# Optimization experiments

Hardware: AMD Instinct MI355X
Metric: run time of the kernel (lower is better)

The kernel has to match this reference:

```python
import jax, jax.numpy as jnp
import numpy as np

NUM_HEADS = 16
ROPE_THETA = 10000.0


def apply_rope(x, positions):
    # x: [B, H, S, D], positions: [S] int
    d = x.shape[-1]
    inv_freq = ROPE_THETA ** (-jnp.arange(0, d, 2, dtype=jnp.float32) / d)  # [D/2]
    ang = positions.astype(jnp.float32)[:, None] * inv_freq[None, :]        # [S, D/2]
    cos, sin = jnp.cos(ang), jnp.sin(ang)                                   # [S, D/2]
    x1, x2 = x[..., 0::2], x[..., 1::2]                                     # even/odd pairs
    r1 = x1 * cos - x2 * sin
    r2 = x1 * sin + x2 * cos
    return jnp.stack([r1, r2], axis=-1).reshape(x.shape)


def setup_inputs() -> dict:
    key = jax.random.key(0)
    k1, k2, k3 = jax.random.split(key, 3)
    B, S, D = 2, 2048, 2048
    x = jax.random.normal(k1, (B, S, D), dtype=jnp.float32)
    token_positions = jnp.arange(S, dtype=jnp.int64)
    w_qkv = jax.random.normal(k2, (D, 3 * D), dtype=jnp.float32) * (D ** -0.5)
    w_o = jax.random.normal(k3, (D, D), dtype=jnp.float32) * (D ** -0.5)
    return {"x": x, "token_positions": token_positions, "w_qkv": w_qkv, "w_o": w_o}


def reference(x, token_positions, w_qkv, w_o):
    B, S, D = x.shape
    H = NUM_HEADS
    hd = D // H
    qkv = x @ w_qkv                                   # [B, S, 3D]
    qkv = qkv.reshape(B, S, 3, H, hd)                 # split '(r h d)'
    q = jnp.transpose(qkv[:, :, 0], (0, 2, 1, 3))     # [B, H, S, hd]
    k = jnp.transpose(qkv[:, :, 1], (0, 2, 1, 3))
    v = jnp.transpose(qkv[:, :, 2], (0, 2, 1, 3))
    q = apply_rope(q, token_positions)
    k = apply_rope(k, token_positions)
    scale = 1.0 / jnp.sqrt(jnp.float32(hd))
    scores = jnp.einsum('bhqd,bhkd->bhqk', q, k) * scale  # [B, H, S, S]
    causal = jnp.tril(jnp.ones((S, S), dtype=bool))
    scores = jnp.where(causal[None, None], scores, jnp.float32(-1e30))
    attn = jax.nn.softmax(scores, axis=-1)
    a = jnp.einsum('bhqk,bhkd->bhqd', attn, v)            # [B, H, S, hd]
    a = jnp.transpose(a, (0, 2, 1, 3)).reshape(B, S, D)   # merge heads, h-major
    return a @ w_o
```

## Files before the change

### kernel.cpp

```cpp
#include <hip/hip_runtime.h>

#define SEQ  2048
#define DIM  2048
#define NH   16
#define HD   128
#define TDIM 6144
#define TT   4096

typedef float  f32x4  __attribute__((ext_vector_type(4)));
typedef __bf16 bf16x8 __attribute__((ext_vector_type(8)));

__device__ __forceinline__ unsigned short f2b(float f){
  union { float f; unsigned int u; } x; x.f = f;
  unsigned int r = x.u + 0x7FFFu + ((x.u >> 16) & 1u);
  return (unsigned short)(r >> 16);
}
__device__ __forceinline__ float b2f(unsigned short b){
  union { unsigned int u; float f; } x; x.u = ((unsigned int)b) << 16;
  return x.f;
}
__device__ __forceinline__ void gl_lds16(const void* g, void* l){
  __builtin_amdgcn_global_load_lds((const __attribute__((address_space(1))) unsigned int*)g,
                                   (__attribute__((address_space(3))) unsigned int*)l, 16, 0, 0);
}

__global__ __launch_bounds__(256) void k_conv(const float* __restrict__ in,
                                              unsigned short* __restrict__ out, int n4){
  int i = blockIdx.x * 256 + threadIdx.x;
  if (i >= n4) return;
  float4 v = ((const float4*)in)[i];
  ushort4 o; o.x = f2b(v.x); o.y = f2b(v.y); o.z = f2b(v.z); o.w = f2b(v.w);
  ((ushort4*)out)[i] = o;
}

__global__ __launch_bounds__(256) void k_tconv(const float* __restrict__ in,
                                               unsigned short* __restrict__ out, int R, int C){
  __shared__ float t[64][33];
  int c0 = blockIdx.x * 32, r0 = blockIdx.y * 64;
  int tx = threadIdx.x & 31, ty = threadIdx.x >> 5;
  for (int i = 0; i < 8; i++)
    t[ty + i*8][tx] = in[(size_t)(r0 + ty + i*8) * C + c0 + tx];
  __syncthreads();
  for (int i = 0; i < 4; i++){
    int c = ty + i*8;
    ushort2 o2; o2.x = f2b(t[2*tx][c]); o2.y = f2b(t[2*tx+1][c]);
    *(ushort2*)&out[(size_t)(c0 + c) * R + r0 + 2*tx] = o2;
  }
}

__global__ __launch_bounds__(256) void k_ropetab(float2* __restrict__ tab){
  int i = blockIdx.x * 256 + threadIdx.x;
  int s = i >> 6, f = i & 63;
  double inv = pow(10000.0, -2.0 * (double)f / 128.0);
  double a = (double)s * inv;
  tab[i] = make_float2((float)cos(a), (float)sin(a));
}

__global__ __launch_bounds__(256) void k_rope(unsigned short* __restrict__ qkv,
                                              const float2* __restrict__ tab){
  int i = blockIdx.x * 256 + threadIdx.x;
  int t   = i >> 11;
  int rem = i & 2047;
  int p   = rem >> 10;
  int pi  = rem & 1023;
  int h   = pi >> 6;
  int f   = pi & 63;
  int s   = t & (SEQ - 1);
  size_t base = (size_t)t * TDIM + p * DIM + h * HD + f * 2;
  unsigned int v = *(const unsigned int*)&qkv[base];
  float x1 = b2f((unsigned short)(v & 0xffffu));
  float x2 = b2f((unsigned short)(v >> 16));
  float2 cs = tab[s * 64 + f];
  float sc2 = (p == 0) ? 0.08838834764831845f : 1.0f;
  float r1 = (x1 * cs.x - x2 * cs.y) * sc2;
  float r2 = (x1 * cs.y + x2 * cs.x) * sc2;
  *(unsigned int*)&qkv[base] = (unsigned int)f2b(r1) | ((unsigned int)f2b(r2) << 16);
}

__global__ __launch_bounds__(256) void k_tv(const unsigned short* __restrict__ qkv,
                                            unsigned short* __restrict__ vT){
  __shared__ unsigned short t[64][65];
  int bh = blockIdx.z; int b = bh >> 4, h = bh & 15;
  const unsigned short* V = qkv + (size_t)b * SEQ * TDIM + 2 * DIM + h * HD;
  unsigned short* o = vT + (size_t)bh * HD * SEQ;
  int s0 = blockIdx.x * 64, d0 = blockIdx.y * 64;
  int tx = threadIdx.x & 31, ty = threadIdx.x >> 5;
  for (int i = 0; i < 8; i++){
    unsigned int v = *(const unsigned int*)&V[(size_t)(s0 + ty + i*8) * TDIM + d0 + 2*tx];
    t[ty + i*8][2*tx]   = (unsigned short)(v & 0xffffu);
    t[ty + i*8][2*tx+1] = (unsigned short)(v >> 16);
  }
  __syncthreads();
  for (int i = 0; i < 8; i++){
    int d = ty + i*8;
    ushort2 o2; o2.x = t[2*tx][d]; o2.y = t[2*tx+1][d];
    *(ushort2*)&o[(size_t)(d0 + d) * SEQ + s0 + 2*tx] = o2;
  }
}

template<bool OUT_F32>
__global__ __launch_bounds__(512, 2) void k_gemm2(const unsigned short* __restrict__ A,
                                                  const unsigned short* __restrict__ BT,
                                                  void* __restrict__ Cout,
                                                  int M, int N, int K){
  __shared__ unsigned short sA[2*2*8192];
  __shared__ unsigned short sB[2*2*8192];
  int tid = threadIdx.x;
  int w = tid >> 6, l = tid & 63;
  int lm = l & 15, lq = l >> 4;
  int wm = w >> 2, wn = w & 3;
  int m0 = blockIdx.y * 256, n0 = blockIdx.x * 256;
  int NT = K >> 6;

  auto stA = [&](int buf, int half, int u){
    unsigned short* dst = sA + (buf*2 + half) * 8192;
    int grow0 = m0 + half*128;
#pragma unroll
    for (int j2 = 0; j2 < 2; j2++){
      int g = j2*512 + tid;
      int r = g >> 3, gc = g & 7;
      gl_lds16(A + (size_t)(grow0 + r) * K + u*64 + ((gc ^ (r & 7)) * 8), dst + g*8);
    }
  };
  auto stB = [&](int buf, int half, int u){
    unsigned short* dst = sB + (buf*2 + half) * 8192;
    int grow0 = n0 + half*128;
#pragma unroll
    for (int j2 = 0; j2 < 2; j2++){
      int g = j2*512 + tid;
      int r = g >> 3, gc = g & 7;
      gl_lds16(BT + (size_t)(grow0 + r) * K + u*64 + ((gc ^ (r & 7)) * 8), dst + g*8);
    }
  };

  f32x4 acc[2][2][4][2] = {};

  stA(0, 0, 0); stB(0, 1, 0); stA(0, 1, 0); stB(0, 0, 0);
  stA(1, 0, 1); stB(1, 1, 1);
  asm volatile("s_waitcnt vmcnt(4)" ::: "memory");
  __builtin_amdgcn_s_barrier();

  for (int t = 0; t < NT; t++){
    int cur = t & 1, nb = cur ^ 1;
    const unsigned short* sAb = sA + cur * 16384;
    const unsigned short* sBb = sB + cur * 16384;
    bf16x8 a[4][2], b0[2][2], b1[2][2];

#pragma unroll
    for (int i = 0; i < 4; i++){
      int r = wm*64 + i*16 + lm;
#pragma unroll
      for (int s = 0; s < 2; s++)
        a[i][s] = *(const bf16x8*)&sAb[r*64 + (((s*4 + lq) ^ (r & 7)) * 8)];
    }
#pragma unroll
    for (int j = 0; j < 2; j++){
      int r = wn*32 + j*16 + lm;
#pragma unroll
      for (int s = 0; s < 2; s++)
        b0[j][s] = *(const bf16x8*)&sBb[r*64 + (((s*4 + lq) ^ (r & 7)) * 8)];
    }
    __builtin_amdgcn_sched_barrier(0);
#pragma unroll
    for (int j = 0; j < 2; j++){
      int r = wn*32 + j*16 + lm;
#pragma unroll
      for (int s = 0; s < 2; s++)
        b1[j][s] = *(const bf16x8*)&sBb[8192 + r*64 + (((s*4 + lq) ^ (r & 7)) * 8)];
    }
    if (t + 1 < NT) stA(nb, 1, t + 1);
    asm volatile("s_waitcnt lgkmcnt(4)" ::: "memory");
    __builtin_amdgcn_sched_barrier(0);
    __builtin_amdgcn_s_setprio(1);
#pragma unroll
    for (int s = 0; s < 2; s++)
#pragma unroll
      for (int i = 0; i < 4; i++)
#pragma unroll
        for (int j = 0; j < 2; j++)
          acc[0][0][i][j] = __builtin_amdgcn_mfma_f32_16x16x32_bf16(a[i][s], b0[j][s],
                                                                    acc[0][0][i][j], 0, 0, 0);
    __builtin_amdgcn_s_setprio(0);
    __builtin_amdgcn_s_barrier();

    if (t + 1 < NT) stB(nb, 0, t + 1);
    asm volatile("s_waitcnt lgkmcnt(0)" ::: "memory");
    __builtin_amdgcn_sched_barrier(0);
    __builtin_amdgcn_s_setprio(1);
#pragma unroll
    for (int s = 0; s < 2; s++)
#pragma unroll
      for (int i = 0; i < 4; i++)
#pragma unroll
        for (int j = 0; j < 2; j++)
          acc[0][1][i][j] = __builtin_amdgcn_mfma_f32_16x16x32_bf16(a[i][s], b1[j][s],
                                                                    acc[0][1][i][j], 0, 0, 0);
    __builtin_amdgcn_s_setprio(0);
#pragma unroll
    for (int i = 0; i < 4; i++){
      int r = wm*64 + i*16 + lm;
#pragma unroll
      for (int s = 0; s < 2; s++)
        a[i][s] = *(const bf16x8*)&sAb[8192 + r*64 + (((s*4 + lq) ^ (r & 7)) * 8)];
    }
    __builtin_amdgcn_s_barrier();

    if (t + 2 < NT) stA(cur, 0, t + 2);
    asm volatile("s_waitcnt lgkmcnt(0)" ::: "memory");
    __builtin_amdgcn_sched_barrier(0);
    __builtin_amdgcn_s_setprio(1);
#pragma unroll
    for (int s = 0; s < 2; s++)
#pragma unroll
      for (int i = 0; i < 4; i++)
#pragma unroll
        for (int j = 0; j < 2; j++)
          acc[1][1][i][j] = __builtin_amdgcn_mfma_f32_16x16x32_bf16(a[i][s], b1[j][s],
                                                                    acc[1][1][i][j], 0, 0, 0);
    __builtin_amdgcn_s_setprio(0);
    __builtin_amdgcn_s_barrier();

    if (t + 2 < NT) stB(cur, 1, t + 2);
    __builtin_amdgcn_s_setprio(1);
#pragma unroll
    for (int s = 0; s < 2; s++)
#pragma unroll
      for (int i = 0; i < 4; i++)
#pragma unroll
        for (int j = 0; j < 2; j++)
          acc[1][0][i][j] = __builtin_amdgcn_mfma_f32_16x16x32_bf16(a[i][s], b0[j][s],
                                                                    acc[1][0][i][j], 0, 0, 0);
    __builtin_amdgcn_s_setprio(0);
    if (t + 2 < NT) asm volatile("s_waitcnt vmcnt(4)" ::: "memory");
    else            asm volatile("s_waitcnt vmcnt(0)" ::: "memory");
    __builtin_amdgcn_s_barrier();
  }

#pragma unroll
  for (int qm = 0; qm < 2; qm++)
#pragma unroll
    for (int qn = 0; qn < 2; qn++)
#pragma unroll
      for (int i = 0; i < 4; i++)
#pragma unroll
        for (int j = 0; j < 2; j++)
#pragma unroll
          for (int r = 0; r < 4; r++){
            int row = m0 + qm*128 + wm*64 + i*16 + lq*4 + r;
            int col = n0 + qn*128 + wn*32 + j*16 + lm;
            float v = acc[qm][qn][i][j][r];
            if (OUT_F32) ((float*)Cout)[(size_t)row * N + col] = v;
            else ((unsigned short*)Cout)[(size_t)row * N + col] = f2b(v);
          }
}

__global__ __launch_bounds__(256, 2) void k_flash(const unsigned short* __restrict__ qkv,
                                                  const unsigned short* __restrict__ vT,
                                                  unsigned short* __restrict__ ab){
  __shared__ unsigned short sK[2][64*128];
  __shared__ unsigned short sV[2][128*64];
  __shared__ unsigned short sP[4][16][68];
  int bh = blockIdx.x; int b = bh >> 4, h = bh & 15;
  int pr = blockIdx.y;
  int tid = threadIdx.x; int w = tid >> 6, l = tid & 63;
  int lm = l & 15, lq = l >> 4;
  const unsigned short* Q  = qkv + (size_t)b * SEQ * TDIM + h * HD;
  const unsigned short* Kp = Q + DIM;
  const unsigned short* Vh = vT + (size_t)bh * HD * SEQ;

  auto stageK = [&](unsigned short* dst, int k0){
    for (int p = 0; p < 4; p++){
      int r = w*16 + p*4 + (l >> 4);
      int g = (l & 15) ^ (r & 15);
      gl_lds16(Kp + (size_t)(k0 + r) * TDIM + g*8, dst + (w*16 + p*4)*128 + l*8);
    }
  };
  auto stageV = [&](unsigned short* dst, int k0){
    for (int p = 0; p < 4; p++){
      int r = w*32 + p*8 + (l >> 3);
      int g = (l & 7) ^ (r & 7);
      gl_lds16(Vh + (size_t)r * SEQ + k0 + g*8, dst + (w*32 + p*8)*64 + l*8);
    }
  };

  for (int seg = 0; seg < 2; seg++){
    int qt = seg ? (31 - pr) : pr;
    int q0 = qt * 64;
    int nkt = qt + 1;

    int qrow = q0 + w*16 + lm;
    bf16x8 qf[4];
    for (int ks = 0; ks < 4; ks++)
      qf[ks] = *(const bf16x8*)&Q[(size_t)qrow * TDIM + ks*32 + lq*8];

    f32x4 o[8] = {};
    float l_i[4] = {0.f, 0.f, 0.f, 0.f};

    stageK(sK[0], 0);
    stageV(sV[0], 0);
    __syncthreads();

    for (int kt = 0; kt < nkt; kt++){
      int cur = kt & 1;
      if (kt + 1 < nkt){
        stageK(sK[cur ^ 1], (kt+1) * 64);
        stageV(sV[cur ^ 1], (kt+1) * 64);
      }
      const unsigned short* sKb = sK[cur];
      const unsigned short* sVb = sV[cur];

      f32x4 sc[4] = {};
      for (int ks = 0; ks < 4; ks++)
        for (int nt = 0; nt < 4; nt++){
          bf16x8 kf = *(const bf16x8*)&sKb[(nt*16 + lm)*128 + (((ks*4 + lq) ^ lm) * 8)];
          sc[nt] = __builtin_amdgcn_mfma_f32_16x16x32_bf16(qf[ks], kf, sc[nt], 0, 0, 0);
        }

      int k0 = kt * 64;
      if (kt == qt){
        for (int nt = 0; nt < 4; nt++)
          for (int r = 0; r < 4; r++){
            float e = __expf(sc[nt][r]);
            if ((k0 + nt*16 + lm) > (q0 + w*16 + lq*4 + r)) e = 0.f;
            l_i[r] += e;
            sP[w][lq*4 + r][nt*16 + lm] = f2b(e);
          }
      } else {
        for (int nt = 0; nt < 4; nt++)
          for (int r = 0; r < 4; r++){
            float e = __expf(sc[nt][r]);
            l_i[r] += e;
            sP[w][lq*4 + r][nt*16 + lm] = f2b(e);
          }
      }

      for (int ks = 0; ks < 2; ks++){
        bf16x8 pf = *(const bf16x8*)&sP[w][lm][ks*32 + lq*8];
        for (int nt = 0; nt < 8; nt++){
          bf16x8 vf = *(const bf16x8*)&sVb[(nt*16 + lm)*64 + (((ks*4 + lq) ^ (lm & 7)) * 8)];
          o[nt] = __builtin_amdgcn_mfma_f32_16x16x32_bf16(pf, vf, o[nt], 0, 0, 0);
        }
      }

      __syncthreads();
    }

    for (int r = 0; r < 4; r++){
      float s = l_i[r];
      for (int d = 1; d < 16; d <<= 1) s += __shfl_xor(s, d, 16);
      float inv = 1.0f / s;
      int trow = b * SEQ + q0 + w*16 + lq*4 + r;
      for (int nt = 0; nt < 8; nt++)
        ab[(size_t)trow * DIM + h * HD + nt*16 + lm] = f2b(o[nt][r] * inv);
    }
  }
}

extern "C" void kernel_launch(void* const* d_in, const int* in_sizes, int n_in,
                              void* d_out, int out_size, void* d_ws, size_t ws_size,
                              hipStream_t stream){
  const float* x     = (const float*)d_in[0];
  const float* w_qkv = (const float*)d_in[2];
  const float* w_o   = (const float*)d_in[3];
  float* out = (float*)d_out;

  char* ws = (char*)d_ws;
  unsigned short* xb    = (unsigned short*)(ws);
  unsigned short* wqkvT = (unsigned short*)(ws + 16777216);
  unsigned short* woT   = (unsigned short*)(ws + 41943040);
  unsigned short* qkvb  = (unsigned short*)(ws + 50331648);
  unsigned short* vTb   = (unsigned short*)(ws + 100663296);
  unsigned short* abb   = (unsigned short*)(ws + 117440512);
  float2*         tab   = (float2*)(ws + 134217728);

  k_conv   <<<8192, 256, 0, stream>>>(x, xb, TT * DIM / 4);
  k_tconv  <<<dim3(TDIM/32, DIM/64), 256, 0, stream>>>(w_qkv, wqkvT, DIM, TDIM);
  k_tconv  <<<dim3(DIM/32,  DIM/64), 256, 0, stream>>>(w_o,   woT,   DIM, DIM);
  k_ropetab<<<SEQ * 64 / 256, 256, 0, stream>>>(tab);
  k_gemm2<false><<<dim3(TDIM/256, TT/256), 512, 0, stream>>>(xb, wqkvT, qkvb, TT, TDIM, DIM);
  k_rope   <<<TT * 2048 / 256, 256, 0, stream>>>(qkvb, tab);
  k_tv     <<<dim3(SEQ/64, HD/64, 32), 256, 0, stream>>>(qkvb, vTb);
  k_flash  <<<dim3(32, 16), 256, 0, stream>>>(qkvb, vTb, abb);
  k_gemm2<true><<<dim3(DIM/256, TT/256), 512, 0, stream>>>(abb, woT, out, TT, DIM, DIM);
}
```

Baseline: 388.7 us.

## Fuse prep kernels, fold RoPE into QKV GEMM epilogue, add narrower output GEMM

Merges the x conversion and RoPE table build into one launch, and both weight transposes into one launch. Applies RoPE and the query scaling inside the QKV GEMM epilogue, using a lane shuffle to fetch the pair partner, which removes the separate RoPE pass over the QKV buffer. Replaces the output projection with a 256x128 tile GEMM so that 256 blocks are launched instead of 128, improving CU fill. Risks include extra epilogue work and table loads in the QKV GEMM, plus a new untested pipelining scheme in the output GEMM.

```diff
diff --git a/kernel.cpp b/kernel.cpp
--- a/kernel.cpp
+++ b/kernel.cpp
@@ -24,19 +24,35 @@
                                    (__attribute__((address_space(3))) unsigned int*)l, 16, 0, 0);
 }
 
-__global__ __launch_bounds__(256) void k_conv(const float* __restrict__ in,
-                                              unsigned short* __restrict__ out, int n4){
-  int i = blockIdx.x * 256 + threadIdx.x;
-  if (i >= n4) return;
-  float4 v = ((const float4*)in)[i];
-  ushort4 o; o.x = f2b(v.x); o.y = f2b(v.y); o.z = f2b(v.z); o.w = f2b(v.w);
-  ((ushort4*)out)[i] = o;
-}
-
-__global__ __launch_bounds__(256) void k_tconv(const float* __restrict__ in,
-                                               unsigned short* __restrict__ out, int R, int C){
+__global__ __launch_bounds__(256) void k_prep(const float* __restrict__ x,
+                                              unsigned short* __restrict__ xb,
+                                              float2* __restrict__ tab){
+  int bid = blockIdx.x;
+  if (bid < 8192){
+    int i = bid * 256 + threadIdx.x;
+    float4 v = ((const float4*)x)[i];
+    ushort4 o; o.x = f2b(v.x); o.y = f2b(v.y); o.z = f2b(v.z); o.w = f2b(v.w);
+    ((ushort4*)xb)[i] = o;
+  } else {
+    int i = (bid - 8192) * 256 + threadIdx.x;
+    int s = i >> 6, f = i & 63;
+    double inv = pow(10000.0, -2.0 * (double)f / 128.0);
+    double a = (double)s * inv;
+    tab[i] = make_float2((float)cos(a), (float)sin(a));
+  }
+}
+
+__global__ __launch_bounds__(256) void k_tconvB(const float* __restrict__ w_qkv,
+                                                unsigned short* __restrict__ wqkvT,
+                                                const float* __restrict__ w_o,
+                                                unsigned short* __restrict__ woT){
+  const float* in; unsigned short* out; int C;
+  if (blockIdx.z == 0){ in = w_qkv; out = wqkvT; C = TDIM; }
+  else                { in = w_o;   out = woT;   C = DIM;  }
+  int c0 = blockIdx.x * 32;
+  if (c0 >= C) return;
   __shared__ float t[64][33];
-  int c0 = blockIdx.x * 32, r0 = blockIdx.y * 64;
+  int r0 = blockIdx.y * 64;
   int tx = threadIdx.x & 31, ty = threadIdx.x >> 5;
   for (int i = 0; i < 8; i++)
     t[ty + i*8][tx] = in[(size_t)(r0 + ty + i*8) * C + c0 + tx];
@@ -44,37 +60,8 @@
   for (int i = 0; i < 4; i++){
     int c = ty + i*8;
     ushort2 o2; o2.x = f2b(t[2*tx][c]); o2.y = f2b(t[2*tx+1][c]);
-    *(ushort2*)&out[(size_t)(c0 + c) * R + r0 + 2*tx] = o2;
-  }
-}
-
-__global__ __launch_bounds__(256) void k_ropetab(float2* __restrict__ tab){
-  int i = blockIdx.x * 256 + threadIdx.x;
-  int s = i >> 6, f = i & 63;
-  double inv = pow(10000.0, -2.0 * (double)f / 128.0);
-  double a = (double)s * inv;
-  tab[i] = make_float2((float)cos(a), (float)sin(a));
-}
-
-__global__ __launch_bounds__(256) void k_rope(unsigned short* __restrict__ qkv,
-                                              const float2* __restrict__ tab){
-  int i = blockIdx.x * 256 + threadIdx.x;
-  int t   = i >> 11;
-  int rem = i & 2047;
-  int p   = rem >> 10;
-  int pi  = rem & 1023;
-  int h   = pi >> 6;
-  int f   = pi & 63;
-  int s   = t & (SEQ - 1);
-  size_t base = (size_t)t * TDIM + p * DIM + h * HD + f * 2;
-  unsigned int v = *(const unsigned int*)&qkv[base];
-  float x1 = b2f((unsigned short)(v & 0xffffu));
-  float x2 = b2f((unsigned short)(v >> 16));
-  float2 cs = tab[s * 64 + f];
-  float sc2 = (p == 0) ? 0.08838834764831845f : 1.0f;
-  float r1 = (x1 * cs.x - x2 * cs.y) * sc2;
-  float r2 = (x1 * cs.y + x2 * cs.x) * sc2;
-  *(unsigned int*)&qkv[base] = (unsigned int)f2b(r1) | ((unsigned int)f2b(r2) << 16);
+    *(ushort2*)&out[(size_t)(c0 + c) * DIM + r0 + 2*tx] = o2;
+  }
 }
 
 __global__ __launch_bounds__(256) void k_tv(const unsigned short* __restrict__ qkv,
@@ -98,11 +85,12 @@
   }
 }
 
-template<bool OUT_F32>
+template<bool OUT_F32, bool ROPE>
 __global__ __launch_bounds__(512, 2) void k_gemm2(const unsigned short* __restrict__ A,
                                                   const unsigned short* __restrict__ BT,
                                                   void* __restrict__ Cout,
-                                                  int M, int N, int K){
+                                                  int M, int N, int K,
+                                                  const float2* __restrict__ tab){
   __shared__ unsigned short sA[2*2*8192];
   __shared__ unsigned short sB[2*2*8192];
   int tid = threadIdx.x;
@@ -196,6 +184,7 @@
           acc[0][1][i][j] = __builtin_amdgcn_mfma_f32_16x16x32_bf16(a[i][s], b1[j][s],
                                                                     acc[0][1][i][j], 0, 0, 0);
     __builtin_amdgcn_s_setprio(0);
+    __builtin_amdgcn_sched_barrier(0);
 #pragma unroll
     for (int i = 0; i < 4; i++){
       int r = wm*64 + i*16 + lm;
@@ -249,9 +238,133 @@
             int row = m0 + qm*128 + wm*64 + i*16 + lq*4 + r;
             int col = n0 + qn*128 + wn*32 + j*16 + lm;
             float v = acc[qm][qn][i][j][r];
+            if (ROPE && col < 2*DIM){
+              float p = __shfl_xor(v, 1);
+              int s_ = row & (SEQ - 1);
+              int f  = (col & 127) >> 1;
+              float2 cs = tab[s_ * 64 + f];
+              float sc2 = (col < DIM) ? 0.08838834764831845f : 1.0f;
+              v = (lm & 1) ? (p * cs.y + v * cs.x) * sc2
+                           : (v * cs.x - p * cs.y) * sc2;
+            }
             if (OUT_F32) ((float*)Cout)[(size_t)row * N + col] = v;
             else ((unsigned short*)Cout)[(size_t)row * N + col] = f2b(v);
           }
+}
+
+__global__ __launch_bounds__(512, 2) void k_gemm3(const unsigned short* __restrict__ A,
+                                                  const unsigned short* __restrict__ BT,
+                                                  float* __restrict__ Cout,
+                                                  int M, int N, int K){
+  __shared__ unsigned short sA[2*2*8192];
+  __shared__ unsigned short sB[2*8192];
+  int tid = threadIdx.x;
+  int w = tid >> 6, l = tid & 63;
+  int lm = l & 15, lq = l >> 4;
+  int wm = w >> 2, wn = w & 3;
+  int m0 = blockIdx.y * 256, n0 = blockIdx.x * 128;
+  int NT = K >> 6;
+
+  auto stA = [&](int buf, int half, int u){
+    unsigned short* dst = sA + (buf*2 + half) * 8192;
+    int grow0 = m0 + half*128;
+#pragma unroll
+    for (int j2 = 0; j2 < 2; j2++){
+      int g = j2*512 + tid;
+      int r = g >> 3, gc = g & 7;
+      gl_lds16(A + (size_t)(grow0 + r) * K + u*64 + ((gc ^ (r & 7)) * 8), dst + g*8);
+    }
+  };
+  auto stB = [&](int buf, int u){
+    unsigned short* dst = sB + buf * 8192;
+#pragma unroll
+    for (int j2 = 0; j2 < 2; j2++){
+      int g = j2*512 + tid;
+      int r = g >> 3, gc = g & 7;
+      gl_lds16(BT + (size_t)(n0 + r) * K + u*64 + ((gc ^ (r & 7)) * 8), dst + g*8);
+    }
+  };
+
+  f32x4 acc[2][4][2] = {};
+
+  stB(0, 0); stA(0, 0, 0); stA(0, 1, 0);
+  asm volatile("s_waitcnt vmcnt(2)" ::: "memory");
+  __builtin_amdgcn_s_barrier();
+
+  for (int t = 0; t < NT; t++){
+    int cur = t & 1, nb = cur ^ 1;
+    const unsigned short* sAb = sA + cur * 16384;
+    const unsigned short* sBb = sB + cur * 8192;
+    bf16x8 a[4][2], b[2][2];
+
+#pragma unroll
+    for (int i = 0; i < 4; i++){
+      int r = wm*64 + i*16 + lm;
+#pragma unroll
+      for (int s = 0; s < 2; s++)
+        a[i][s] = *(const bf16x8*)&sAb[r*64 + (((s*4 + lq) ^ (r & 7)) * 8)];
+    }
+#pragma unroll
+    for (int j = 0; j < 2; j++){
+      int r = wn*32 + j*16 + lm;
+#pragma unroll
+      for (int s = 0; s < 2; s++)
+        b[j][s] = *(const bf16x8*)&sBb[r*64 + (((s*4 + lq) ^ (r & 7)) * 8)];
+    }
+    if (t + 1 < NT){ stB(nb, t + 1); stA(nb, 0, t + 1); }
+    asm volatile("s_waitcnt lgkmcnt(0)" ::: "memory");
+    __builtin_amdgcn_sched_barrier(0);
+    __builtin_amdgcn_s_setprio(1);
+#pragma unroll
+    for (int s = 0; s < 2; s++)
+#pragma unroll
+      for (int i = 0; i < 4; i++)
+#pragma unroll
+        for (int j = 0; j < 2; j++)
+          acc[0][i][j] = __builtin_amdgcn_mfma_f32_16x16x32_bf16(a[i][s], b[j][s],
+                                                                 acc[0][i][j], 0, 0, 0);
+    __builtin_amdgcn_s_setprio(0);
+    if (t + 1 < NT) asm volatile("s_waitcnt vmcnt(4)" ::: "memory");
+    else            asm volatile("s_waitcnt vmcnt(0)" ::: "memory");
+    __builtin_amdgcn_s_barrier();
+
+#pragma unroll
+    for (int i = 0; i < 4; i++){
+      int r = wm*64 + i*16 + lm;
+#pragma unroll
+      for (int s = 0; s < 2; s++)
+        a[i][s] = *(const bf16x8*)&sAb[8192 + r*64 + (((s*4 + lq) ^ (r & 7)) * 8)];
+    }
+    if (t + 1 < NT) stA(nb, 1, t + 1);
+    asm volatile("s_waitcnt lgkmcnt(0)" ::: "memory");
+    __builtin_amdgcn_sched_barrier(0);
+    __builtin_amdgcn_s_setprio(1);
+#pragma unroll
+    for (int s = 0; s < 2; s++)
+#pragma unroll
+      for (int i = 0; i < 4; i++)
+#pragma unroll
+        for (int j = 0; j < 2; j++)
+          acc[1][i][j] = __builtin_amdgcn_mfma_f32_16x16x32_bf16(a[i][s], b[j][s],
+                                                                 acc[1][i][j], 0, 0, 0);
+    __builtin_amdgcn_s_setprio(0);
+    if (t + 1 < NT) asm volatile("s_waitcnt vmcnt(2)" ::: "memory");
+    else            asm volatile("s_waitcnt vmcnt(0)" ::: "memory");
+    __builtin_amdgcn_s_barrier();
+  }
+
+#pragma unroll
+  for (int qm = 0; qm < 2; qm++)
+#pragma unroll
+    for (int i = 0; i < 4; i++)
+#pragma unroll
+      for (int j = 0; j < 2; j++)
+#pragma unroll
+        for (int r = 0; r < 4; r++){
+          int row = m0 + qm*128 + wm*64 + i*16 + lq*4 + r;
+          int col = n0 + wn*32 + j*16 + lm;
+          Cout[(size_t)row * N + col] = acc[qm][i][j][r];
+        }
 }
 
 __global__ __launch_bounds__(256, 2) void k_flash(const unsigned short* __restrict__ qkv,
@@ -373,13 +486,11 @@
   unsigned short* abb   = (unsigned short*)(ws + 117440512);
   float2*         tab   = (float2*)(ws + 134217728);
 
-  k_conv   <<<8192, 256, 0, stream>>>(x, xb, TT * DIM / 4);
-  k_tconv  <<<dim3(TDIM/32, DIM/64), 256, 0, stream>>>(w_qkv, wqkvT, DIM, TDIM);
-  k_tconv  <<<dim3(DIM/32,  DIM/64), 256, 0, stream>>>(w_o,   woT,   DIM, DIM);
-  k_ropetab<<<SEQ * 64 / 256, 256, 0, stream>>>(tab);
-  k_gemm2<false><<<dim3(TDIM/256, TT/256), 512, 0, stream>>>(xb, wqkvT, qkvb, TT, TDIM, DIM);
-  k_rope   <<<TT * 2048 / 256, 256, 0, stream>>>(qkvb, tab);
+  k_prep   <<<8704, 256, 0, stream>>>(x, xb, tab);
+  k_tconvB <<<dim3(TDIM/32, DIM/64, 2), 256, 0, stream>>>(w_qkv, wqkvT, w_o, woT);
+  k_gemm2<false,true><<<dim3(TDIM/256, TT/256), 512, 0, stream>>>(xb, wqkvT, qkvb,
+                                                                  TT, TDIM, DIM, tab);
   k_tv     <<<dim3(SEQ/64, HD/64, 32), 256, 0, stream>>>(qkvb, vTb);
   k_flash  <<<dim3(32, 16), 256, 0, stream>>>(qkvb, vTb, abb);
-  k_gemm2<true><<<dim3(DIM/256, TT/256), 512, 0, stream>>>(abb, woT, out, TT, DIM, DIM);
-}
+  k_gemm3  <<<dim3(DIM/128, TT/256), 512, 0, stream>>>(abb, woT, out, TT, DIM, DIM);
+}
```

Result: slower. 400.9 us (+3.2%).
